# Kernel optimization log

Hardware: AMD Instinct MI355X
Metric: run time of the kernel (lower is better)

## Reference

```python
import jax, jax.numpy as jnp
import numpy as np

NEG_SLOPE = 0.2  # PyG GATConv default negative_slope


def _gat_layer(x, src, dst, W_src, W_dst, att_src, att_dst, bias, num_nodes):
    """Single-head GATConv (concat=True, heads=1, add_self_loops=False)."""
    h_src = x @ W_src                      # [N, C]
    h_dst = x @ W_dst                      # [N, C]
    a_src = h_src @ att_src                # [N]
    a_dst = h_dst @ att_dst                # [N]
    # per-edge attention logits: message j -> i uses a_src[j] + a_dst[i]
    e = jax.nn.leaky_relu(a_src[src] + a_dst[dst], NEG_SLOPE)  # [E]
    # numerically stable softmax over incoming edges of each destination
    m = jax.ops.segment_max(e, dst, num_segments=num_nodes)    # [N]
    ee = jnp.exp(e - m[dst])                                   # [E]
    denom = jax.ops.segment_sum(ee, dst, num_segments=num_nodes)  # [N]
    alpha = ee / denom[dst]                                    # [E]
    # attention-weighted scatter-add of source messages
    out = jax.ops.segment_sum(h_src[src] * alpha[:, None], dst,
                              num_segments=num_nodes)          # [N, C]
    return out + bias


def setup_inputs() -> dict:
    key = jax.random.key(0)
    ks = jax.random.split(key, 12)
    N, E, F_IN, HID, OUT = 100000, 1600000, 128, 128, 64
    inp = {
        "x": jax.random.normal(ks[0], (N, F_IN), dtype=jnp.float32),
        "edge_index": jax.random.randint(ks[1], (2, E), 0, N, dtype=jnp.int64
                                         if jax.config.jax_enable_x64 else jnp.int32),
        "W_src1": jax.random.normal(ks[2], (F_IN, HID), dtype=jnp.float32) / np.sqrt(F_IN),
        "W_dst1": jax.random.normal(ks[3], (F_IN, HID), dtype=jnp.float32) / np.sqrt(F_IN),
        "att_src1": jax.random.normal(ks[4], (HID,), dtype=jnp.float32) / np.sqrt(HID),
        "att_dst1": jax.random.normal(ks[5], (HID,), dtype=jnp.float32) / np.sqrt(HID),
        "b1": jnp.zeros((HID,), dtype=jnp.float32),
        "W_src2": jax.random.normal(ks[6], (HID, OUT), dtype=jnp.float32) / np.sqrt(HID),
        "W_dst2": jax.random.normal(ks[7], (HID, OUT), dtype=jnp.float32) / np.sqrt(HID),
        "att_src2": jax.random.normal(ks[8], (OUT,), dtype=jnp.float32) / np.sqrt(OUT),
        "att_dst2": jax.random.normal(ks[9], (OUT,), dtype=jnp.float32) / np.sqrt(OUT),
        "b2": jnp.zeros((OUT,), dtype=jnp.float32),
    }
    return inp


def reference(x, edge_index, W_src1, W_dst1, att_src1, att_dst1, b1,
              W_src2, W_dst2, att_src2, att_dst2, b2):
    N = x.shape[0]
    src, dst = edge_index[0], edge_index[1]
    h = _gat_layer(x, src, dst, W_src1, W_dst1, att_src1, att_dst1, b1, N)
    h = jax.nn.relu(h)
    out = _gat_layer(h, src, dst, W_src2, W_dst2, att_src2, att_dst2, b2, N)
    return out
```

## Files before the change

kernel.cpp:

```cpp
#include <hip/hip_runtime.h>

#define F_IN 128
#define NEG_SLOPE 0.2f
#define SCAN_CHUNK 2048
#define CH 4096

typedef __attribute__((ext_vector_type(8))) short bf16x8;
typedef __attribute__((ext_vector_type(4))) float f32x4;

__device__ inline unsigned short f2bf(float f) {
    unsigned int u = __float_as_uint(f);
    unsigned int r = (u + 0x7fffu + ((u >> 16) & 1u)) >> 16;
    return (unsigned short)r;
}
__device__ inline float bf2f(unsigned short h) { return __uint_as_float((unsigned int)h << 16); }
__device__ inline float bflo(unsigned int u) { return __uint_as_float(u << 16); }
__device__ inline float bfhi(unsigned int u) { return __uint_as_float(u & 0xffff0000u); }

__device__ inline int bswiz(int n, int k) {
    int ct = n >> 4, rlo = n & 15, kk = k >> 5, q = (k >> 3) & 3, j = k & 7;
    return (((ct * 4 + kk) * 64 + q * 16 + rlo) << 3) + j;
}

__global__ void k_prep(const float* __restrict__ Ws1, const float* __restrict__ Wd1,
                       const float* __restrict__ as1, const float* __restrict__ ad1,
                       const float* __restrict__ Ws2, const float* __restrict__ Wd2,
                       const float* __restrict__ as2, const float* __restrict__ ad2,
                       float* __restrict__ vecs,
                       unsigned short* __restrict__ w1hi, unsigned short* __restrict__ w1lo,
                       unsigned short* __restrict__ w2hi, unsigned short* __restrict__ w2lo) {
    int bid = blockIdx.x, tid = threadIdx.x;
    if (bid == 0 && tid < 128) {
        int f = tid;
        float s1 = 0.f, d1 = 0.f, s2 = 0.f, d2 = 0.f;
        for (int c = 0; c < 128; ++c) {
            s1 += Ws1[f * 128 + c] * as1[c];
            d1 += Wd1[f * 128 + c] * ad1[c];
        }
        for (int c = 0; c < 64; ++c) {
            s2 += Ws2[f * 64 + c] * as2[c];
            d2 += Wd2[f * 64 + c] * ad2[c];
        }
        vecs[f] = s1; vecs[128 + f] = d1; vecs[256 + f] = s2; vecs[384 + f] = d2;
    } else if (bid >= 1 && bid < 65) {
        int idx = (bid - 1) * 256 + tid;
        int n = idx >> 7, k = idx & 127;
        float w = Ws1[k * 128 + n];
        unsigned short h = f2bf(w);
        int si = bswiz(n, k);
        w1hi[si] = h;
        w1lo[si] = f2bf(w - bf2f(h));
    } else if (bid >= 65 && bid < 97) {
        int idx = (bid - 65) * 256 + tid;
        int n = idx >> 7, k = idx & 127;
        float w = Ws2[k * 64 + n];
        unsigned short h = f2bf(w);
        int si = bswiz(n, k);
        w2hi[si] = h;
        w2lo[si] = f2bf(w - bf2f(h));
    }
}


__global__ void k_bhist(const int* __restrict__ dsts, int* __restrict__ table,
                        int E, int NB, int nblk) {
    __shared__ int bins[512];
    int t = threadIdx.x, blk = blockIdx.x;
    for (int j = t; j < NB; j += 256) bins[j] = 0;
    __syncthreads();
    int base = blk * CH;
    #pragma unroll
    for (int k = 0; k < CH / 256; ++k) {
        int idx = base + k * 256 + t;
        if (idx < E) atomicAdd(&bins[dsts[idx] >> 8], 1);
    }
    __syncthreads();
    for (int j = t; j < NB; j += 256) table[(long long)j * nblk + blk] = bins[j];
}

__global__ void k_blocksum2(const int* __restrict__ in, int* __restrict__ bsum, int M) {
    __shared__ int sh[256];
    int t = threadIdx.x;
    long long base = (long long)blockIdx.x * SCAN_CHUNK + (long long)t * 8;
    int s = 0;
    #pragma unroll
    for (int k = 0; k < 8; ++k) {
        long long i = base + k;
        if (i < M) s += in[i];
    }
    sh[t] = s;
    __syncthreads();
    for (int off = 128; off; off >>= 1) {
        if (t < off) sh[t] += sh[t + off];
        __syncthreads();
    }
    if (t == 0) bsum[blockIdx.x] = sh[0];
}

__global__ void k_scan2(int* __restrict__ io, const int* __restrict__ bsum, int M) {
    __shared__ int sh[256];
    int t = threadIdx.x, bid = blockIdx.x;
    int pre = 0;
    for (int b = 0; b < bid; ++b) pre += bsum[b];
    long long base = (long long)bid * SCAN_CHUNK + (long long)t * 8;
    int loc[8];
    int s = 0;
    #pragma unroll
    for (int k = 0; k < 8; ++k) {
        long long i = base + k;
        int v = (i < M) ? io[i] : 0;
        loc[k] = s;
        s += v;
    }
    sh[t] = s;
    __syncthreads();
    for (int off = 1; off < 256; off <<= 1) {
        int tmp = (t >= off) ? sh[t - off] : 0;
        __syncthreads();
        sh[t] += tmp;
        __syncthreads();
    }
    int toff = pre + sh[t] - s;
    #pragma unroll
    for (int k = 0; k < 8; ++k) {
        long long i = base + k;
        if (i < M) io[i] = toff + loc[k];
    }
}

__global__ void k_bscat(const int* __restrict__ srcs, const int* __restrict__ dsts,
                        const int* __restrict__ table, int* __restrict__ pairA,
                        int E, int NB, int nblk) {
    __shared__ int offs[512];
    int t = threadIdx.x, blk = blockIdx.x;
    for (int j = t; j < NB; j += 256) offs[j] = table[(long long)j * nblk + blk];
    __syncthreads();
    int base = blk * CH;
    #pragma unroll
    for (int k = 0; k < CH / 256; ++k) {
        int idx = base + k * 256 + t;
        if (idx < E) {
            int d = dsts[idx], s = srcs[idx];
            int p = atomicAdd(&offs[d >> 8], 1);
            pairA[p] = (s << 8) | (d & 255);
        }
    }
}

__global__ void k_bfin(const int* __restrict__ pairA, const int* __restrict__ table,
                       int* __restrict__ perm, int* __restrict__ rowptr,
                       int NB, int nblk, int N, int E) {
    __shared__ int scnt[256];
    __shared__ int sh[256];
    __shared__ int sptr[256];
    int t = threadIdx.x, b = blockIdx.x;
    int beg = table[(long long)b * nblk];
    int end = (b + 1 < NB) ? table[(long long)(b + 1) * nblk] : E;
    scnt[t] = 0;
    __syncthreads();
    for (int i = beg + t; i < end; i += 256) {
        atomicAdd(&scnt[pairA[i] & 255], 1);
    }
    __syncthreads();
    int c = scnt[t];
    sh[t] = c;
    __syncthreads();
    for (int off = 1; off < 256; off <<= 1) {
        int tmp = (t >= off) ? sh[t - off] : 0;
        __syncthreads();
        sh[t] += tmp;
        __syncthreads();
    }
    int excl = sh[t] - c;
    int node = (b << 8) + t;
    if (node < N) rowptr[node] = beg + excl;
    sptr[t] = beg + excl;
    __syncthreads();
    for (int i = beg + t; i < end; i += 256) {
        int u = pairA[i];
        int pos = atomicAdd(&sptr[u & 255], 1);
        perm[pos] = u >> 8;
    }
    if (b == NB - 1 && t == 0) rowptr[N] = E;
}

__launch_bounds__(256)
__global__ void k_alpha(const int* __restrict__ rowptr, const int* __restrict__ perm,
                        const float* __restrict__ a_s, const float* __restrict__ a_d,
                        float* __restrict__ w, int N) {
    long long wid = ((long long)blockIdx.x * 256 + threadIdx.x) >> 6;
    int lane = threadIdx.x & 63;
    int g = lane >> 4, l = lane & 15;
    long long row = wid * 4 + g;
    if (row >= N) return;
    int beg = rowptr[row], end = rowptr[row + 1];
    float ad = a_d[row];
    for (int i = beg + l; i < end; i += 16) {
        float t = a_s[perm[i]] + ad;
        t = t > 0.f ? t : NEG_SLOPE * t;
        w[i] = __expf(t);
    }
}

template <int COLS, bool ABF16>
__launch_bounds__(256)
__global__ void k_gemm_mfma(const void* __restrict__ Xv,
                            const unsigned short* __restrict__ Bh,
                            const unsigned short* __restrict__ Bl,
                            const float* __restrict__ vecs_s,
                            const float* __restrict__ vecs_d,
                            unsigned short* __restrict__ H,
                            float* __restrict__ a_s, float* __restrict__ a_d, int N) {
    int tid = threadIdx.x;
    int wave = tid >> 6, lane = tid & 63;
    int q = lane >> 4, rlo = lane & 15;
    long long wrow0 = (long long)blockIdx.x * 128 + wave * 32;

    bf16x8 Ahi[2][4], Alo[2][4];
    #pragma unroll
    for (int rt = 0; rt < 2; ++rt) {
        long long r = wrow0 + rt * 16 + rlo;
        long long rr = (r < N) ? r : (long long)(N - 1);
        float ps = 0.f, pd = 0.f;
        #pragma unroll
        for (int kk = 0; kk < 4; ++kk) {
            int k0 = kk * 32 + q * 8;
            float xv[8];
            if constexpr (ABF16) {
                const unsigned short* Xu = (const unsigned short*)Xv;
                bf16x8 av = *(const bf16x8*)(Xu + rr * 128 + k0);
                Ahi[rt][kk] = av;
                #pragma unroll
                for (int j = 0; j < 8; ++j) xv[j] = bf2f((unsigned short)av[j]);
            } else {
                const float* Xf = (const float*)Xv;
                float4 x0 = *(const float4*)(Xf + rr * 128 + k0);
                float4 x1 = *(const float4*)(Xf + rr * 128 + k0 + 4);
                xv[0] = x0.x; xv[1] = x0.y; xv[2] = x0.z; xv[3] = x0.w;
                xv[4] = x1.x; xv[5] = x1.y; xv[6] = x1.z; xv[7] = x1.w;
                bf16x8 ah, al;
                #pragma unroll
                for (int j = 0; j < 8; ++j) {
                    unsigned short h = f2bf(xv[j]);
                    ah[j] = (short)h;
                    al[j] = (short)f2bf(xv[j] - bf2f(h));
                }
                Ahi[rt][kk] = ah; Alo[rt][kk] = al;
            }
            float4 vs0 = *(const float4*)(vecs_s + k0);
            float4 vs1 = *(const float4*)(vecs_s + k0 + 4);
            float4 vd0 = *(const float4*)(vecs_d + k0);
            float4 vd1 = *(const float4*)(vecs_d + k0 + 4);
            ps += xv[0] * vs0.x + xv[1] * vs0.y + xv[2] * vs0.z + xv[3] * vs0.w
                + xv[4] * vs1.x + xv[5] * vs1.y + xv[6] * vs1.z + xv[7] * vs1.w;
            pd += xv[0] * vd0.x + xv[1] * vd0.y + xv[2] * vd0.z + xv[3] * vd0.w
                + xv[4] * vd1.x + xv[5] * vd1.y + xv[6] * vd1.z + xv[7] * vd1.w;
        }
        ps += __shfl_xor(ps, 16); ps += __shfl_xor(ps, 32);
        pd += __shfl_xor(pd, 16); pd += __shfl_xor(pd, 32);
        if (q == 0 && r < N) { a_s[r] = ps; a_d[r] = pd; }
    }

    const bf16x8* Bh8 = (const bf16x8*)Bh;
    const bf16x8* Bl8 = (const bf16x8*)Bl;
    #pragma unroll 1
    for (int ct = 0; ct < COLS / 16; ++ct) {
        bf16x8 bh[4], bl[4];
        #pragma unroll
        for (int kk = 0; kk < 4; ++kk) {
            bh[kk] = Bh8[(ct * 4 + kk) * 64 + lane];
            bl[kk] = Bl8[(ct * 4 + kk) * 64 + lane];
        }
        f32x4 acc0 = {0.f, 0.f, 0.f, 0.f};
        f32x4 acc1 = {0.f, 0.f, 0.f, 0.f};
        #pragma unroll
        for (int kk = 0; kk < 4; ++kk) {
            acc0 = __builtin_amdgcn_mfma_f32_16x16x32_bf16(Ahi[0][kk], bh[kk], acc0, 0, 0, 0);
            acc1 = __builtin_amdgcn_mfma_f32_16x16x32_bf16(Ahi[1][kk], bh[kk], acc1, 0, 0, 0);
            if constexpr (!ABF16) {
                acc0 = __builtin_amdgcn_mfma_f32_16x16x32_bf16(Alo[0][kk], bh[kk], acc0, 0, 0, 0);
                acc1 = __builtin_amdgcn_mfma_f32_16x16x32_bf16(Alo[1][kk], bh[kk], acc1, 0, 0, 0);
            }
            acc0 = __builtin_amdgcn_mfma_f32_16x16x32_bf16(Ahi[0][kk], bl[kk], acc0, 0, 0, 0);
            acc1 = __builtin_amdgcn_mfma_f32_16x16x32_bf16(Ahi[1][kk], bl[kk], acc1, 0, 0, 0);
        }
        #pragma unroll
        for (int i2 = 0; i2 < 4; ++i2) {
            long long o0 = wrow0 + q * 4 + i2;
            long long o1 = wrow0 + 16 + q * 4 + i2;
            if (o0 < N) H[o0 * COLS + ct * 16 + rlo] = f2bf(acc0[i2]);
            if (o1 < N) H[o1 * COLS + ct * 16 + rlo] = f2bf(acc1[i2]);
        }
    }
}

__launch_bounds__(256)
__global__ void k_agg128(const int* __restrict__ rowptr, const int* __restrict__ perm,
                         const float* __restrict__ wbuf,
                         const unsigned short* __restrict__ H, const float* __restrict__ bias,
                         unsigned short* __restrict__ out_bf, int N) {
    int wave = (int)(((long long)blockIdx.x * 256 + threadIdx.x) >> 6);
    int lane = threadIdx.x & 63;
    if (wave >= N) return;
    int beg = __builtin_amdgcn_readfirstlane(rowptr[wave]);
    int end = __builtin_amdgcn_readfirstlane(rowptr[wave + 1]);

    const unsigned int* H32 = (const unsigned int*)H;
    float acc0 = 0.f, acc1 = 0.f, wsum = 0.f;
    int i = beg;
    for (; i + 16 <= end; i += 16) {
        int s[16];
        float wv[16];
        unsigned int v[16];
        #pragma unroll
        for (int j = 0; j < 16; ++j)
            s[j] = __builtin_amdgcn_readfirstlane(perm[i + j]);
        #pragma unroll
        for (int j = 0; j < 16; ++j)
            wv[j] = wbuf[i + j];
        #pragma unroll
        for (int j = 0; j < 16; ++j)
            v[j] = H32[(long long)s[j] * 64 + lane];
        #pragma unroll
        for (int j = 0; j < 16; ++j) {
            acc0 += wv[j] * bflo(v[j]);
            acc1 += wv[j] * bfhi(v[j]);
            wsum += wv[j];
        }
    }
    for (; i + 8 <= end; i += 8) {
        int s[8];
        float wv[8];
        unsigned int v[8];
        #pragma unroll
        for (int j = 0; j < 8; ++j)
            s[j] = __builtin_amdgcn_readfirstlane(perm[i + j]);
        #pragma unroll
        for (int j = 0; j < 8; ++j)
            wv[j] = wbuf[i + j];
        #pragma unroll
        for (int j = 0; j < 8; ++j)
            v[j] = H32[(long long)s[j] * 64 + lane];
        #pragma unroll
        for (int j = 0; j < 8; ++j) {
            acc0 += wv[j] * bflo(v[j]);
            acc1 += wv[j] * bfhi(v[j]);
            wsum += wv[j];
        }
    }
    for (; i < end; ++i) {
        int s = __builtin_amdgcn_readfirstlane(perm[i]);
        float w = wbuf[i];
        unsigned int v = H32[(long long)s * 64 + lane];
        acc0 += w * bflo(v); acc1 += w * bfhi(v);
        wsum += w;
    }
    float inv = (wsum > 0.f) ? __fdividef(1.f, wsum) : 0.f;
    float o0 = fmaxf(acc0 * inv + bias[2 * lane], 0.f);
    float o1 = fmaxf(acc1 * inv + bias[2 * lane + 1], 0.f);
    unsigned int pk = (unsigned int)f2bf(o0) | ((unsigned int)f2bf(o1) << 16);
    ((unsigned int*)out_bf)[(long long)wave * 64 + lane] = pk;
}

__launch_bounds__(256)
__global__ void k_agg64(const int* __restrict__ rowptr, const int* __restrict__ perm,
                        const float* __restrict__ wbuf,
                        const unsigned short* __restrict__ H, const float* __restrict__ bias,
                        float* __restrict__ out, int N) {
    int wave = (int)(((long long)blockIdx.x * 256 + threadIdx.x) >> 6);
    int lane = threadIdx.x & 63;
    if (wave >= N) return;
    int c = lane & 31, h = lane >> 5;
    int beg = __builtin_amdgcn_readfirstlane(rowptr[wave]);
    int end = __builtin_amdgcn_readfirstlane(rowptr[wave + 1]);

    const unsigned int* H32 = (const unsigned int*)H;
    float acc0 = 0.f, acc1 = 0.f, wsum = 0.f;
    int base = beg;
    for (; base + 16 <= end; base += 16) {
        int s[8];
        float wv[8];
        unsigned int v[8];
        #pragma unroll
        for (int j = 0; j < 8; ++j)
            s[j] = perm[base + h + 2 * j];
        #pragma unroll
        for (int j = 0; j < 8; ++j)
            wv[j] = wbuf[base + h + 2 * j];
        #pragma unroll
        for (int j = 0; j < 8; ++j)
            v[j] = H32[(long long)s[j] * 32 + c];
        #pragma unroll
        for (int j = 0; j < 8; ++j) {
            acc0 += wv[j] * bflo(v[j]);
            acc1 += wv[j] * bfhi(v[j]);
            wsum += wv[j];
        }
    }
    for (; base + 8 <= end; base += 8) {
        int s[4];
        float wv[4];
        unsigned int v[4];
        #pragma unroll
        for (int j = 0; j < 4; ++j)
            s[j] = perm[base + h + 2 * j];
        #pragma unroll
        for (int j = 0; j < 4; ++j)
            wv[j] = wbuf[base + h + 2 * j];
        #pragma unroll
        for (int j = 0; j < 4; ++j)
            v[j] = H32[(long long)s[j] * 32 + c];
        #pragma unroll
        for (int j = 0; j < 4; ++j) {
            acc0 += wv[j] * bflo(v[j]);
            acc1 += wv[j] * bfhi(v[j]);
            wsum += wv[j];
        }
    }
    for (int i = base + h; i < end; i += 2) {
        int s = perm[i];
        float w = wbuf[i];
        unsigned int v = H32[(long long)s * 32 + c];
        acc0 += w * bflo(v); acc1 += w * bfhi(v);
        wsum += w;
    }
    acc0 += __shfl_xor(acc0, 32);
    acc1 += __shfl_xor(acc1, 32);
    wsum += __shfl_xor(wsum, 32);
    if (h == 0) {
        float inv = (wsum > 0.f) ? __fdividef(1.f, wsum) : 0.f;
        float2 o;
        o.x = acc0 * inv + bias[2 * c];
        o.y = acc1 * inv + bias[2 * c + 1];
        *(float2*)(out + (long long)wave * 64 + 2 * c) = o;
    }
}

extern "C" void kernel_launch(void* const* d_in, const int* in_sizes, int n_in,
                              void* d_out, int out_size, void* d_ws, size_t ws_size,
                              hipStream_t stream) {
    const float* x   = (const float*)d_in[0];
    const int*   ei  = (const int*)d_in[1];
    const float* Ws1 = (const float*)d_in[2];
    const float* Wd1 = (const float*)d_in[3];
    const float* as1 = (const float*)d_in[4];
    const float* ad1 = (const float*)d_in[5];
    const float* b1  = (const float*)d_in[6];
    const float* Ws2 = (const float*)d_in[7];
    const float* Wd2 = (const float*)d_in[8];
    const float* as2 = (const float*)d_in[9];
    const float* ad2 = (const float*)d_in[10];
    const float* b2  = (const float*)d_in[11];
    float* out = (float*)d_out;

    const int N = in_sizes[0] / F_IN;
    const int E = in_sizes[1] / 2;
    const int* srcs = ei;
    const int* dsts = ei + E;

    const int nblk = (E + CH - 1) / CH;
    const int NB   = (N + 255) >> 8;
    const int M    = NB * nblk;
    const int nb2  = (M + SCAN_CHUNK - 1) / SCAN_CHUNK;

    unsigned short* hbuf = (unsigned short*)d_ws;
    unsigned short* x2bf = hbuf + (size_t)N * 128;
    int*   perm   = (int*)(x2bf + (size_t)N * 128);
    float* a_s1   = (float*)(perm + E);
    float* a_d1   = a_s1 + N;
    float* a_s2   = a_d1 + N;
    float* a_d2   = a_s2 + N;
    float* wbuf   = a_d2 + N;
    int*   rowptr = (int*)(wbuf + E);
    int*   bsum   = rowptr + N + 4;
    unsigned short* w1hi = (unsigned short*)(bsum + 128);
    unsigned short* w1lo = w1hi + 16384;
    unsigned short* w2hi = w1lo + 16384;
    unsigned short* w2lo = w2hi + 8192;
    float* vecs   = (float*)(w2lo + 8192);
    int*   pairA  = (int*)x2bf;
    int*   table  = pairA + E;

    k_prep<<<97, 256, 0, stream>>>(Ws1, Wd1, as1, ad1, Ws2, Wd2, as2, ad2,
                                   vecs, w1hi, w1lo, w2hi, w2lo);
    k_bhist<<<nblk, 256, 0, stream>>>(dsts, table, E, NB, nblk);
    k_blocksum2<<<nb2, 256, 0, stream>>>(table, bsum, M);
    k_scan2<<<nb2, 256, 0, stream>>>(table, bsum, M);
    k_bscat<<<nblk, 256, 0, stream>>>(srcs, dsts, table, pairA, E, NB, nblk);
    k_bfin<<<NB, 256, 0, stream>>>(pairA, table, perm, rowptr, NB, nblk, N, E);

    const int ablocks = (((N + 3) / 4) * 64 + 255) / 256;

    k_gemm_mfma<128, false><<<(N + 127) / 128, 256, 0, stream>>>(
        x, w1hi, w1lo, vecs, vecs + 128, hbuf, a_s1, a_d1, N);
    k_alpha<<<ablocks, 256, 0, stream>>>(rowptr, perm, a_s1, a_d1, wbuf, N);
    k_agg128<<<(N + 3) / 4, 256, 0, stream>>>(
        rowptr, perm, wbuf, hbuf, b1, x2bf, N);

    k_gemm_mfma<64, true><<<(N + 127) / 128, 256, 0, stream>>>(
        x2bf, w2hi, w2lo, vecs + 256, vecs + 384, hbuf, a_s2, a_d2, N);
    k_alpha<<<ablocks, 256, 0, stream>>>(rowptr, perm, a_s2, a_d2, wbuf, N);
    k_agg64<<<(N + 3) / 4, 256, 0, stream>>>(
        rowptr, perm, wbuf, hbuf, b2, out, N);
}
```

Before: 345.5 us.

## Fuse edge attention weight computation into aggregation kernels

```diff
diff --git a/kernel.cpp b/kernel.cpp
--- a/kernel.cpp
+++ b/kernel.cpp
@@ -182,24 +182,6 @@
         perm[pos] = u >> 8;
     }
     if (b == NB - 1 && t == 0) rowptr[N] = E;
-}
-
-__launch_bounds__(256)
-__global__ void k_alpha(const int* __restrict__ rowptr, const int* __restrict__ perm,
-                        const float* __restrict__ a_s, const float* __restrict__ a_d,
-                        float* __restrict__ w, int N) {
-    long long wid = ((long long)blockIdx.x * 256 + threadIdx.x) >> 6;
-    int lane = threadIdx.x & 63;
-    int g = lane >> 4, l = lane & 15;
-    long long row = wid * 4 + g;
-    if (row >= N) return;
-    int beg = rowptr[row], end = rowptr[row + 1];
-    float ad = a_d[row];
-    for (int i = beg + l; i < end; i += 16) {
-        float t = a_s[perm[i]] + ad;
-        t = t > 0.f ? t : NEG_SLOPE * t;
-        w[i] = __expf(t);
-    }
 }
 
 template <int COLS, bool ABF16>
@@ -296,7 +278,7 @@
 
 __launch_bounds__(256)
 __global__ void k_agg128(const int* __restrict__ rowptr, const int* __restrict__ perm,
-                         const float* __restrict__ wbuf,
+                         const float* __restrict__ a_s, const float* __restrict__ a_d,
                          const unsigned short* __restrict__ H, const float* __restrict__ bias,
                          unsigned short* __restrict__ out_bf, int N) {
     int wave = (int)(((long long)blockIdx.x * 256 + threadIdx.x) >> 6);
@@ -304,54 +286,57 @@
     if (wave >= N) return;
     int beg = __builtin_amdgcn_readfirstlane(rowptr[wave]);
     int end = __builtin_amdgcn_readfirstlane(rowptr[wave + 1]);
+    float ad = __uint_as_float(__builtin_amdgcn_readfirstlane(__float_as_uint(a_d[wave])));
 
     const unsigned int* H32 = (const unsigned int*)H;
     float acc0 = 0.f, acc1 = 0.f, wsum = 0.f;
     int i = beg;
     for (; i + 16 <= end; i += 16) {
-        int s[16];
-        float wv[16];
+        int pl = perm[i + (lane & 15)];
+        float t = a_s[pl] + ad;
+        t = t > 0.f ? t : NEG_SLOPE * t;
+        float wl = __expf(t);
         unsigned int v[16];
         #pragma unroll
-        for (int j = 0; j < 16; ++j)
-            s[j] = __builtin_amdgcn_readfirstlane(perm[i + j]);
-        #pragma unroll
-        for (int j = 0; j < 16; ++j)
-            wv[j] = wbuf[i + j];
-        #pragma unroll
-        for (int j = 0; j < 16; ++j)
-            v[j] = H32[(long long)s[j] * 64 + lane];
-        #pragma unroll
         for (int j = 0; j < 16; ++j) {
-            acc0 += wv[j] * bflo(v[j]);
-            acc1 += wv[j] * bfhi(v[j]);
-            wsum += wv[j];
+            int sj = __builtin_amdgcn_readlane(pl, j);
+            v[j] = H32[(long long)sj * 64 + lane];
+        }
+        #pragma unroll
+        for (int j = 0; j < 16; ++j) {
+            float wj = __uint_as_float(
+                (unsigned int)__builtin_amdgcn_readlane((int)__float_as_uint(wl), j));
+            acc0 += wj * bflo(v[j]);
+            acc1 += wj * bfhi(v[j]);
+            wsum += wj;
         }
     }
     for (; i + 8 <= end; i += 8) {
-        int s[8];
-        float wv[8];
+        int pl = perm[i + (lane & 7)];
+        float t = a_s[pl] + ad;
+        t = t > 0.f ? t : NEG_SLOPE * t;
+        float wl = __expf(t);
         unsigned int v[8];
         #pragma unroll
-        for (int j = 0; j < 8; ++j)
-            s[j] = __builtin_amdgcn_readfirstlane(perm[i + j]);
-        #pragma unroll
-        for (int j = 0; j < 8; ++j)
-            wv[j] = wbuf[i + j];
-        #pragma unroll
-        for (int j = 0; j < 8; ++j)
-            v[j] = H32[(long long)s[j] * 64 + lane];
-        #pragma unroll
         for (int j = 0; j < 8; ++j) {
-            acc0 += wv[j] * bflo(v[j]);
-            acc1 += wv[j] * bfhi(v[j]);
-            wsum += wv[j];
+            int sj = __builtin_amdgcn_readlane(pl, j);
+            v[j] = H32[(long long)sj * 64 + lane];
+        }
+        #pragma unroll
+        for (int j = 0; j < 8; ++j) {
+            float wj = __uint_as_float(
+                (unsigned int)__builtin_amdgcn_readlane((int)__float_as_uint(wl), j));
+            acc0 += wj * bflo(v[j]);
+            acc1 += wj * bfhi(v[j]);
+            wsum += wj;
         }
     }
     for (; i < end; ++i) {
         int s = __builtin_amdgcn_readfirstlane(perm[i]);
-        float w = wbuf[i];
         unsigned int v = H32[(long long)s * 64 + lane];
+        float t = a_s[s] + ad;
+        t = t > 0.f ? t : NEG_SLOPE * t;
+        float w = __expf(t);
         acc0 += w * bflo(v); acc1 += w * bfhi(v);
         wsum += w;
     }
@@ -364,7 +349,7 @@
 
 __launch_bounds__(256)
 __global__ void k_agg64(const int* __restrict__ rowptr, const int* __restrict__ perm,
-                        const float* __restrict__ wbuf,
+                        const float* __restrict__ a_s, const float* __restrict__ a_d,
                         const unsigned short* __restrict__ H, const float* __restrict__ bias,
                         float* __restrict__ out, int N) {
     int wave = (int)(((long long)blockIdx.x * 256 + threadIdx.x) >> 6);
@@ -373,23 +358,27 @@
     int c = lane & 31, h = lane >> 5;
     int beg = __builtin_amdgcn_readfirstlane(rowptr[wave]);
     int end = __builtin_amdgcn_readfirstlane(rowptr[wave + 1]);
+    float ad = __uint_as_float(__builtin_amdgcn_readfirstlane(__float_as_uint(a_d[wave])));
 
     const unsigned int* H32 = (const unsigned int*)H;
     float acc0 = 0.f, acc1 = 0.f, wsum = 0.f;
     int base = beg;
     for (; base + 16 <= end; base += 16) {
-        int s[8];
+        int pl = perm[base + (lane & 15)];
+        float t = a_s[pl] + ad;
+        t = t > 0.f ? t : NEG_SLOPE * t;
+        float wl = __expf(t);
+        int sv[8];
         float wv[8];
         unsigned int v[8];
         #pragma unroll
+        for (int j = 0; j < 8; ++j) {
+            sv[j] = __shfl(pl, h + 2 * j);
+            wv[j] = __shfl(wl, h + 2 * j);
+        }
+        #pragma unroll
         for (int j = 0; j < 8; ++j)
-            s[j] = perm[base + h + 2 * j];
-        #pragma unroll
-        for (int j = 0; j < 8; ++j)
-            wv[j] = wbuf[base + h + 2 * j];
-        #pragma unroll
-        for (int j = 0; j < 8; ++j)
-            v[j] = H32[(long long)s[j] * 32 + c];
+            v[j] = H32[(long long)sv[j] * 32 + c];
         #pragma unroll
         for (int j = 0; j < 8; ++j) {
             acc0 += wv[j] * bflo(v[j]);
@@ -398,18 +387,21 @@
         }
     }
     for (; base + 8 <= end; base += 8) {
-        int s[4];
+        int pl = perm[base + (lane & 7)];
+        float t = a_s[pl] + ad;
+        t = t > 0.f ? t : NEG_SLOPE * t;
+        float wl = __expf(t);
+        int sv[4];
         float wv[4];
         unsigned int v[4];
         #pragma unroll
+        for (int j = 0; j < 4; ++j) {
+            sv[j] = __shfl(pl, h + 2 * j);
+            wv[j] = __shfl(wl, h + 2 * j);
+        }
+        #pragma unroll
         for (int j = 0; j < 4; ++j)
-            s[j] = perm[base + h + 2 * j];
-        #pragma unroll
-        for (int j = 0; j < 4; ++j)
-            wv[j] = wbuf[base + h + 2 * j];
-        #pragma unroll
-        for (int j = 0; j < 4; ++j)
-            v[j] = H32[(long long)s[j] * 32 + c];
+            v[j] = H32[(long long)sv[j] * 32 + c];
         #pragma unroll
         for (int j = 0; j < 4; ++j) {
             acc0 += wv[j] * bflo(v[j]);
@@ -419,8 +411,10 @@
     }
     for (int i = base + h; i < end; i += 2) {
         int s = perm[i];
-        float w = wbuf[i];
         unsigned int v = H32[(long long)s * 32 + c];
+        float t = a_s[s] + ad;
+        t = t > 0.f ? t : NEG_SLOPE * t;
+        float w = __expf(t);
         acc0 += w * bflo(v); acc1 += w * bfhi(v);
         wsum += w;
     }
@@ -470,8 +464,7 @@
     float* a_d1   = a_s1 + N;
     float* a_s2   = a_d1 + N;
     float* a_d2   = a_s2 + N;
-    float* wbuf   = a_d2 + N;
-    int*   rowptr = (int*)(wbuf + E);
+    int*   rowptr = (int*)(a_d2 + N);
     int*   bsum   = rowptr + N + 4;
     unsigned short* w1hi = (unsigned short*)(bsum + 128);
     unsigned short* w1lo = w1hi + 16384;
@@ -489,17 +482,13 @@
     k_bscat<<<nblk, 256, 0, stream>>>(srcs, dsts, table, pairA, E, NB, nblk);
     k_bfin<<<NB, 256, 0, stream>>>(pairA, table, perm, rowptr, NB, nblk, N, E);
 
-    const int ablocks = (((N + 3) / 4) * 64 + 255) / 256;
-
     k_gemm_mfma<128, false><<<(N + 127) / 128, 256, 0, stream>>>(
         x, w1hi, w1lo, vecs, vecs + 128, hbuf, a_s1, a_d1, N);
-    k_alpha<<<ablocks, 256, 0, stream>>>(rowptr, perm, a_s1, a_d1, wbuf, N);
     k_agg128<<<(N + 3) / 4, 256, 0, stream>>>(
-        rowptr, perm, wbuf, hbuf, b1, x2bf, N);
+        rowptr, perm, a_s1, a_d1, hbuf, b1, x2bf, N);
 
     k_gemm_mfma<64, true><<<(N + 127) / 128, 256, 0, stream>>>(
         x2bf, w2hi, w2lo, vecs + 256, vecs + 384, hbuf, a_s2, a_d2, N);
-    k_alpha<<<ablocks, 256, 0, stream>>>(rowptr, perm, a_s2, a_d2, wbuf, N);
     k_agg64<<<(N + 3) / 4, 256, 0, stream>>>(
-        rowptr, perm, wbuf, hbuf, b2, out, N);
-}
+        rowptr, perm, a_s2, a_d2, hbuf, b2, out, N);
+}
```

Measured after the change: 319.3 us. 1.08x faster.
